# Kernel tuning notes

Measured on AMD Instinct MI355X. Metric: run time of the kernel, lower is better.

The kernel has to match this reference:

```python
import jax, jax.numpy as jnp
import numpy as np

B, N, M = 8, 8192, 2048
C1, C2 = 128, 256
H = 256  # mlp hidden/out channels


def setup_inputs() -> dict:
    key = jax.random.key(0)
    ks = jax.random.split(key, 8)
    return {
        "unknown": jax.random.normal(ks[0], (B, N, 3), dtype=jnp.float32),
        "known": jax.random.normal(ks[1], (B, M, 3), dtype=jnp.float32),
        "unknow_feats": jax.random.normal(ks[2], (B, C1, N), dtype=jnp.float32),
        "known_feats": jax.random.normal(ks[3], (B, C2, M), dtype=jnp.float32),
        "W1": jax.random.normal(ks[4], (H, C1 + C2), dtype=jnp.float32) * 0.02,
        "b1": jnp.zeros((H,), dtype=jnp.float32),
        "W2": jax.random.normal(ks[5], (H, H), dtype=jnp.float32) * 0.02,
        "b2": jnp.zeros((H,), dtype=jnp.float32),
    }


def _three_nn(unknown, known):
    # squared pairwise distances (B, n, m)
    d2 = jnp.sum((unknown[:, :, None, :] - known[:, None, :, :]) ** 2, axis=-1)
    neg_d2_top, idx = jax.lax.top_k(-d2, 3)  # 3 smallest distances
    dist = jnp.sqrt(jnp.maximum(-neg_d2_top, 0.0))  # (B, n, 3)
    return dist, idx


def _three_interpolate(features, idx, weight):
    # features: (B, c, m); idx, weight: (B, n, 3) -> (B, c, n)
    Bc, c, m = features.shape
    n = idx.shape[1]
    idx_flat = jnp.broadcast_to(idx.reshape(Bc, 1, n * 3), (Bc, c, n * 3))
    gathered = jnp.take_along_axis(features, idx_flat, axis=2).reshape(Bc, c, n, 3)
    return jnp.sum(gathered * weight[:, None, :, :], axis=-1)


def reference(unknown, known, unknow_feats, known_feats, W1, b1, W2, b2):
    dist, idx = _three_nn(unknown, known)
    dist_recip = 1.0 / (dist + 1e-8)
    weight = dist_recip / jnp.sum(dist_recip, axis=2, keepdims=True)  # (B, n, 3)
    interpolated = _three_interpolate(known_feats, idx, weight)  # (B, C2, n)
    new_features = jnp.concatenate([interpolated, unknow_feats], axis=1)  # (B, C1+C2, n)
    # shared MLP: two conv1x1 (bias, no BN) + ReLU
    h = jax.nn.relu(jnp.einsum('oc,bcn->bon', W1, new_features) + b1[None, :, None])
    out = jax.nn.relu(jnp.einsum('oc,bcn->bon', W2, h) + b2[None, :, None])
    return out
```

## Files before the change

### kernel.cpp

```cpp
#include <hip/hip_runtime.h>

using bf16x8 = __attribute__((ext_vector_type(8))) short;
using f32x4  = __attribute__((ext_vector_type(4))) float;
using f32x2  = __attribute__((ext_vector_type(2))) float;

constexpr int Bb = 8, Nn = 8192, Mm = 2048, C1 = 128, C2 = 256, Hh = 256, K1 = 384;
constexpr int KT1 = K1 / 32;
constexpr int KT2 = Hh / 32;
constexpr int RT = Hh / 16;
constexpr int NQ = 4;
constexpr int MQ = Mm / NQ;

__device__ __forceinline__ short f2bf(float x) {
  union { float f; unsigned u; } v; v.f = x;
  unsigned r = v.u + 0x7fff + ((v.u >> 16) & 1);
  return (short)(r >> 16);
}

__device__ __forceinline__ unsigned pk2bf(float a, float b) {
#if defined(__has_builtin) && __has_builtin(__builtin_amdgcn_cvt_pk_bf16_f32)
  typedef __attribute__((ext_vector_type(2))) __bf16 bf2_t;
  bf2_t r = __builtin_amdgcn_cvt_pk_bf16_f32(a, b);
  union { bf2_t v; unsigned u; } cvt; cvt.v = r;
  return cvt.u;
#else
  return (unsigned)(unsigned short)f2bf(a) | ((unsigned)(unsigned short)f2bf(b) << 16);
#endif
}

__device__ __forceinline__ float bflo(unsigned d) { return __uint_as_float(d << 16); }
__device__ __forceinline__ float bfhi(unsigned d) { return __uint_as_float(d & 0xffff0000u); }

__device__ __forceinline__ f32x2 pk_add(f32x2 a, f32x2 b) {
  f32x2 d; asm("v_pk_add_f32 %0, %1, %2" : "=v"(d) : "v"(a), "v"(b)); return d;
}
__device__ __forceinline__ f32x2 pk_mul(f32x2 a, f32x2 b) {
  f32x2 d; asm("v_pk_mul_f32 %0, %1, %2" : "=v"(d) : "v"(a), "v"(b)); return d;
}
__device__ __forceinline__ f32x2 pk_fma(f32x2 a, f32x2 b, f32x2 c) {
  f32x2 d; asm("v_pk_fma_f32 %0, %1, %2, %3" : "=v"(d) : "v"(a), "v"(b), "v"(c)); return d;
}

__device__ __forceinline__ void merge3(float a0, float a1, float a2, int A0, int A1, int A2,
                                       float b0, float b1, float b2, int B0, int B1, int B2,
                                       float& m0, float& m1, float& m2,
                                       int& j0, int& j1, int& j2) {
  bool ta = a0 <= b0;
  m0 = ta ? a0 : b0; j0 = ta ? A0 : B0;
  float na0 = ta ? a1 : a0, na1 = ta ? a2 : a1;
  int   nA0 = ta ? A1 : A0, nA1 = ta ? A2 : A1;
  float nb0 = ta ? b0 : b1, nb1 = ta ? b1 : b2;
  int   nB0 = ta ? B0 : B1, nB1 = ta ? B1 : B2;
  ta = na0 <= nb0;
  m1 = ta ? na0 : nb0; j1 = ta ? nA0 : nB0;
  float ma0 = ta ? na1 : na0; int mA0 = ta ? nA1 : nA0;
  float mb0 = ta ? nb0 : nb1; int mB0 = ta ? nB0 : nB1;
  ta = ma0 <= mb0;
  m2 = ta ? ma0 : mb0; j2 = ta ? mA0 : mB0;
}

__global__ __launch_bounds__(256) void prep_all_k(const float* __restrict__ kf,
                                                  short* __restrict__ kfTb,
                                                  const float* __restrict__ W1,
                                                  const float* __restrict__ W2,
                                                  short* __restrict__ W1f,
                                                  short* __restrict__ W2f) {
  __shared__ float tile[32][33];
  int bid = blockIdx.x, tid = threadIdx.x;
  if (bid < 4096) {
    int cx = bid & 63, ry = (bid >> 6) & 7, z = bid >> 9;
    const float* src = kf + (size_t)z * C2 * Mm;
    short* dst = kfTb + (size_t)z * Mm * C2;
    int c0 = cx * 32, r0 = ry * 32;
    int tx = tid & 31, ty = tid >> 5;
#pragma unroll
    for (int rr = ty; rr < 32; rr += 8)
      tile[rr][tx] = src[(size_t)(r0 + rr) * Mm + c0 + tx];
    __syncthreads();
#pragma unroll
    for (int cc = ty; cc < 32; cc += 8)
      dst[(size_t)(c0 + cc) * C2 + r0 + tx] = f2bf(tile[tx][cc]);
    return;
  }
  int id = (bid - 4096) * 256 + tid;
  const int n1 = KT1 * RT * 64;
  const int n2 = KT2 * RT * 64;
  if (id < n1) {
    int lane = id & 63, t = id >> 6;
    int kt = t / RT, rt = t % RT;
    int m = rt * 16 + (lane & 15), k0 = kt * 32 + (lane >> 4) * 8;
    bf16x8 f;
#pragma unroll
    for (int j = 0; j < 8; ++j) f[j] = f2bf(W1[(size_t)m * K1 + k0 + j]);
    *(bf16x8*)(W1f + (size_t)id * 8) = f;
  } else if (id < n1 + n2) {
    int id2 = id - n1;
    int lane = id2 & 63, t = id2 >> 6;
    int kt = t / RT, rt = t % RT;
    int m = rt * 16 + (lane & 15), k0 = kt * 32 + (lane >> 4) * 8;
    bf16x8 f;
#pragma unroll
    for (int j = 0; j < 8; ++j) f[j] = f2bf(W2[(size_t)m * Hh + k0 + j]);
    *(bf16x8*)(W2f + (size_t)id2 * 8) = f;
  }
}

__global__ __launch_bounds__(256) void nn_quarter_k(const float* __restrict__ unknown,
                                                    const float* __restrict__ known,
                                                    float* __restrict__ pd,
                                                    int* __restrict__ pi) {
  __shared__ float kx[MQ], ky[MQ], kz[MQ];
  int bid = blockIdx.x;
  int b = bid >> 7, rem = bid & 127;
  int q = rem & 3, nblk = rem >> 2;
  int n = nblk * 256 + threadIdx.x;
  const float* kb = known + ((size_t)b * Mm + q * MQ) * 3;
  for (int p = threadIdx.x; p < MQ; p += 256) {
    kx[p] = kb[3 * p]; ky[p] = kb[3 * p + 1]; kz[p] = kb[3 * p + 2];
  }
  __syncthreads();

  size_t ui = ((size_t)b * Nn + n) * 3;
  float ux = unknown[ui], uy = unknown[ui + 1], uz = unknown[ui + 2];
  float d0 = 1e30f, d1 = 1e30f, d2 = 1e30f;
  int i0 = 0, i1 = 0, i2 = 0;
  int gbase = q * MQ;

  f32x2 nux = { -ux, -ux }, nuy = { -uy, -uy }, nuz = { -uz, -uz };

#define NN_INS(dd, qq)                                                  \
  {                                                                     \
    if (__any((dd) < d2)) {  \
      int jm = gbase + jb + (qq);                                       \
      bool c0 = (dd) < d0, c1 = (dd) < d1, c2 = (dd) < d2;              \
      d2 = c1 ? d1 : (c2 ? (dd) : d2); i2 = c1 ? i1 : (c2 ? jm : i2);   \
      d1 = c0 ? d0 : (c1 ? (dd) : d1); i1 = c0 ? i0 : (c1 ? jm : i1);   \
      d0 = c0 ? (dd) : d0;             i0 = c0 ? jm : i0;               \
    }                                                                   \
  }

  const f32x2* kx2 = (const f32x2*)kx;
  const f32x2* ky2 = (const f32x2*)ky;
  const f32x2* kz2 = (const f32x2*)kz;
  for (int jb = 0; jb < MQ; jb += 4) {
    int h = jb >> 1;
    f32x2 xa = kx2[h], xb = kx2[h + 1];
    f32x2 ya = ky2[h], yb = ky2[h + 1];
    f32x2 za = kz2[h], zb = kz2[h + 1];
    f32x2 dxa = pk_add(xa, nux), dya = pk_add(ya, nuy), dza = pk_add(za, nuz);
    f32x2 dda = pk_fma(dza, dza, pk_fma(dya, dya, pk_mul(dxa, dxa)));
    f32x2 dxb = pk_add(xb, nux), dyb = pk_add(yb, nuy), dzb = pk_add(zb, nuz);
    f32x2 ddb = pk_fma(dzb, dzb, pk_fma(dyb, dyb, pk_mul(dxb, dxb)));
    NN_INS(dda.x, 0)
    NN_INS(dda.y, 1)
    NN_INS(ddb.x, 2)
    NN_INS(ddb.y, 3)
  }
#undef NN_INS

  size_t o = (((size_t)b * Nn + n) * NQ + q) * 3;
  pd[o] = d0; pd[o + 1] = d1; pd[o + 2] = d2;
  pi[o] = i0; pi[o + 1] = i1; pi[o + 2] = i2;
}

__global__ __launch_bounds__(256) void fused_gemm_k(
    const float* __restrict__ uf, const short* __restrict__ kfTb,
    const short* __restrict__ W1f, const float* __restrict__ b1,
    const short* __restrict__ W2f, const float* __restrict__ b2,
    const float* __restrict__ pd, const int* __restrict__ pi,
    float* __restrict__ out) {
  __shared__ short Fs[KT2 * 4 * 64 * 8];
  short* Hs = Fs;
  int bid = blockIdx.x;
  int b = bid >> 7, bt = bid & 127;
  int tid = threadIdx.x, lane = tid & 63, wv = tid >> 6;
  int quad = lane >> 4, col = lane & 15;
  const int nq = bt * 64 + wv * 16 + col;

  float w0, w1, w2;
  int g0, g1, g2;
  {
    size_t pbase = (size_t)(b * Nn + nq) * (NQ * 3);
    float4 da = *(const float4*)&pd[pbase];
    float4 db = *(const float4*)&pd[pbase + 4];
    float4 dc = *(const float4*)&pd[pbase + 8];
    int4 ia = *(const int4*)&pi[pbase];
    int4 ib = *(const int4*)&pi[pbase + 4];
    int4 ic = *(const int4*)&pi[pbase + 8];
    float t0, t1, t2, u0, u1, u2, m0, m1, m2;
    int T0, T1, T2, U0, U1, U2;
    merge3(da.x, da.y, da.z, ia.x, ia.y, ia.z,
           da.w, db.x, db.y, ia.w, ib.x, ib.y, t0, t1, t2, T0, T1, T2);
    merge3(db.z, db.w, dc.x, ib.z, ib.w, ic.x,
           dc.y, dc.z, dc.w, ic.y, ic.z, ic.w, u0, u1, u2, U0, U1, U2);
    merge3(t0, t1, t2, T0, T1, T2, u0, u1, u2, U0, U1, U2,
           m0, m1, m2, g0, g1, g2);
    float s0 = sqrtf(m0), s1 = sqrtf(m1), s2 = sqrtf(m2);
    float r0 = 1.f / (s0 + 1e-8f), r1 = 1.f / (s1 + 1e-8f), r2 = 1.f / (s2 + 1e-8f);
    float rs = 1.f / (r0 + r1 + r2);
    w0 = r0 * rs; w1 = r1 * rs; w2 = r2 * rs;
  }
  const short* kfb = kfTb + (size_t)b * Mm * C2;

#define PACK_STORE(q0, q1, q2, plane)                                         \
  {                                                                           \
    float e0 = w0 * bflo((q0).x) + w1 * bflo((q1).x) + w2 * bflo((q2).x);     \
    float e1 = w0 * bfhi((q0).x) + w1 * bfhi((q1).x) + w2 * bfhi((q2).x);     \
    float e2 = w0 * bflo((q0).y) + w1 * bflo((q1).y) + w2 * bflo((q2).y);     \
    float e3 = w0 * bfhi((q0).y) + w1 * bfhi((q1).y) + w2 * bfhi((q2).y);     \
    float e4 = w0 * bflo((q0).z) + w1 * bflo((q1).z) + w2 * bflo((q2).z);     \
    float e5 = w0 * bfhi((q0).z) + w1 * bfhi((q1).z) + w2 * bfhi((q2).z);     \
    float e6 = w0 * bflo((q0).w) + w1 * bflo((q1).w) + w2 * bflo((q2).w);     \
    float e7 = w0 * bfhi((q0).w) + w1 * bfhi((q1).w) + w2 * bfhi((q2).w);     \
    uint4 packed;                                                             \
    packed.x = pk2bf(e0, e1); packed.y = pk2bf(e2, e3);                       \
    packed.z = pk2bf(e4, e5); packed.w = pk2bf(e6, e7);                       \
    *(uint4*)&Fs[(((plane) * 4 + wv) * 64 + lane) * 8] = packed;              \
  }

#define GATHER_KT(kt, plane)                                                  \
  {                                                                           \
    int c0 = (kt) * 32 + quad * 8;                                            \
    uint4 q0 = *(const uint4*)&kfb[(size_t)g0 * C2 + c0];                     \
    uint4 q1 = *(const uint4*)&kfb[(size_t)g1 * C2 + c0];                     \
    uint4 q2 = *(const uint4*)&kfb[(size_t)g2 * C2 + c0];                     \
    PACK_STORE(q0, q1, q2, plane)                                             \
  }

#pragma unroll 3
  for (int kt = 0; kt < 6; ++kt) GATHER_KT(kt, kt)
  __syncthreads();

  uint4 pf0, pf1, pf2, pf3, pf4, pf5;
  {
    int c06 = 6 * 32 + quad * 8, c07 = 7 * 32 + quad * 8;
    pf0 = *(const uint4*)&kfb[(size_t)g0 * C2 + c06];
    pf1 = *(const uint4*)&kfb[(size_t)g1 * C2 + c06];
    pf2 = *(const uint4*)&kfb[(size_t)g2 * C2 + c06];
    pf3 = *(const uint4*)&kfb[(size_t)g0 * C2 + c07];
    pf4 = *(const uint4*)&kfb[(size_t)g1 * C2 + c07];
    pf5 = *(const uint4*)&kfb[(size_t)g2 * C2 + c07];
  }

  f32x4 acc[4][4];
#pragma unroll
  for (int r = 0; r < 4; ++r)
#pragma unroll
    for (int c = 0; c < 4; ++c) acc[r][c] = (f32x4){0.f, 0.f, 0.f, 0.f};

  for (int kt = 0; kt < 6; ++kt) {
    bf16x8 Afr[4], Bfr[4];
#pragma unroll
    for (int r = 0; r < 4; ++r)
      Afr[r] = *(const bf16x8*)(W1f + ((size_t)(kt * RT + wv * 4 + r) * 64 + lane) * 8);
#pragma unroll
    for (int c = 0; c < 4; ++c)
      Bfr[c] = *(const bf16x8*)&Fs[((kt * 4 + c) * 64 + lane) * 8];
#pragma unroll
    for (int r = 0; r < 4; ++r)
#pragma unroll
      for (int c = 0; c < 4; ++c)
        acc[r][c] = __builtin_amdgcn_mfma_f32_16x16x32_bf16(Afr[r], Bfr[c], acc[r][c], 0, 0, 0);
  }
  __syncthreads();

  float eu[4][8];
#pragma unroll
  for (int kt = 8; kt < 12; ++kt) {
    int c1 = (kt - 8) * 32 + quad * 8;
#pragma unroll
    for (int j = 0; j < 8; ++j)
      eu[kt - 8][j] = uf[((size_t)b * C1 + c1 + j) * Nn + nq];
  }
  PACK_STORE(pf0, pf1, pf2, 0)
  PACK_STORE(pf3, pf4, pf5, 1)
#pragma unroll
  for (int kt = 8; kt < 12; ++kt) {
    uint4 packed;
    packed.x = pk2bf(eu[kt - 8][0], eu[kt - 8][1]);
    packed.y = pk2bf(eu[kt - 8][2], eu[kt - 8][3]);
    packed.z = pk2bf(eu[kt - 8][4], eu[kt - 8][5]);
    packed.w = pk2bf(eu[kt - 8][6], eu[kt - 8][7]);
    *(uint4*)&Fs[(((kt - 6) * 4 + wv) * 64 + lane) * 8] = packed;
  }
#undef GATHER_KT
#undef PACK_STORE
  __syncthreads();

  for (int kt = 6; kt < KT1; ++kt) {
    bf16x8 Afr[4], Bfr[4];
#pragma unroll
    for (int r = 0; r < 4; ++r)
      Afr[r] = *(const bf16x8*)(W1f + ((size_t)(kt * RT + wv * 4 + r) * 64 + lane) * 8);
#pragma unroll
    for (int c = 0; c < 4; ++c)
      Bfr[c] = *(const bf16x8*)&Fs[(((kt - 6) * 4 + c) * 64 + lane) * 8];
#pragma unroll
    for (int r = 0; r < 4; ++r)
#pragma unroll
      for (int c = 0; c < 4; ++c)
        acc[r][c] = __builtin_amdgcn_mfma_f32_16x16x32_bf16(Afr[r], Bfr[c], acc[r][c], 0, 0, 0);
  }

#pragma unroll
  for (int r = 0; r < 4; ++r) {
    f32x4 bq = *(const f32x4*)&b1[wv * 64 + r * 16 + quad * 4];
#pragma unroll
    for (int c = 0; c < 4; ++c)
#pragma unroll
      for (int reg = 0; reg < 4; ++reg)
        acc[r][c][reg] = fmaxf(acc[r][c][reg] + bq[reg], 0.f);
  }
  __syncthreads();
  {
    int addr_lo = (((quad & 1) * 2) * 16 + col) * 4;
    bool hiSel = lane >= 32;
#pragma unroll
    for (int ktl = 0; ktl < 2; ++ktl)
#pragma unroll
      for (int c = 0; c < 4; ++c) {
        float e[8];
#pragma unroll
        for (int j = 0; j < 8; ++j) {
          int addr = addr_lo + (j >> 2) * 64;
          int lo = __builtin_amdgcn_ds_bpermute(addr, __float_as_int(acc[ktl * 2][c][j & 3]));
          int hi = __builtin_amdgcn_ds_bpermute(addr, __float_as_int(acc[ktl * 2 + 1][c][j & 3]));
          e[j] = __int_as_float(hiSel ? hi : lo);
        }
        uint4 packed;
        packed.x = pk2bf(e[0], e[1]); packed.y = pk2bf(e[2], e[3]);
        packed.z = pk2bf(e[4], e[5]); packed.w = pk2bf(e[6], e[7]);
        *(uint4*)&Hs[(((wv * 2 + ktl) * 4 + c) * 64 + lane) * 8] = packed;
      }
  }
  __syncthreads();

  f32x4 acc2[4][4];
#pragma unroll
  for (int r = 0; r < 4; ++r)
#pragma unroll
    for (int c = 0; c < 4; ++c) acc2[r][c] = (f32x4){0.f, 0.f, 0.f, 0.f};

  for (int kt = 0; kt < KT2; ++kt) {
    bf16x8 Afr[4], Bfr[4];
#pragma unroll
    for (int r = 0; r < 4; ++r)
      Afr[r] = *(const bf16x8*)(W2f + ((size_t)(kt * RT + wv * 4 + r) * 64 + lane) * 8);
#pragma unroll
    for (int c = 0; c < 4; ++c)
      Bfr[c] = *(const bf16x8*)&Hs[((kt * 4 + c) * 64 + lane) * 8];
#pragma unroll
    for (int r = 0; r < 4; ++r)
#pragma unroll
      for (int c = 0; c < 4; ++c)
        acc2[r][c] = __builtin_amdgcn_mfma_f32_16x16x32_bf16(Afr[r], Bfr[c], acc2[r][c], 0, 0, 0);
  }

#pragma unroll
  for (int r = 0; r < 4; ++r) {
    f32x4 bq = *(const f32x4*)&b2[wv * 64 + r * 16 + quad * 4];
#pragma unroll
    for (int c = 0; c < 4; ++c)
#pragma unroll
      for (int reg = 0; reg < 4; ++reg) {
        int rowg = wv * 64 + r * 16 + quad * 4 + reg;
        int n = bt * 64 + c * 16 + col;
        out[((size_t)b * Hh + rowg) * Nn + n] = fmaxf(acc2[r][c][reg] + bq[reg], 0.f);
      }
  }
}

extern "C" void kernel_launch(void* const* d_in, const int* in_sizes, int n_in,
                              void* d_out, int out_size, void* d_ws, size_t ws_size,
                              hipStream_t stream) {
  const float* unknown = (const float*)d_in[0];
  const float* known   = (const float*)d_in[1];
  const float* uf      = (const float*)d_in[2];
  const float* kf      = (const float*)d_in[3];
  const float* W1      = (const float*)d_in[4];
  const float* b1      = (const float*)d_in[5];
  const float* W2      = (const float*)d_in[6];
  const float* b2      = (const float*)d_in[7];
  float* out = (float*)d_out;

  char* p = (char*)d_ws;
  short* kfTb = (short*)p; p += (size_t)Bb * Mm * C2 * 2;
  short* W1f = (short*)p;  p += (size_t)KT1 * RT * 64 * 8 * 2;
  short* W2f = (short*)p;  p += (size_t)KT2 * RT * 64 * 8 * 2;
  float* pd  = (float*)p;  p += (size_t)Bb * Nn * NQ * 3 * 4;
  int* pi    = (int*)p;    p += (size_t)Bb * Nn * NQ * 3 * 4;

  const int prep_blocks = 4096 + (KT1 * RT * 64 + KT2 * RT * 64 + 255) / 256;
  prep_all_k<<<dim3(prep_blocks), dim3(256), 0, stream>>>(kf, kfTb, W1, W2, W1f, W2f);
  nn_quarter_k<<<dim3(Bb * 32 * NQ), dim3(256), 0, stream>>>(unknown, known, pd, pi);
  fused_gemm_k<<<dim3(Bb * (Nn / 64)), dim3(256), 0, stream>>>(
      uf, kfTb, W1f, b1, W2f, b2, pd, pi, out);
}
```

Measured before the change: 214.8 us.

## Restructure first GEMM into three 4-tile stages overlapping gathers with MFMA

The layer-1 K loop is reordered into three stages of four k-tiles. The unknown-feature tiles are loaded first and multiplied while the register-prefetched gathers for the first half of the interpolated channels are in flight. The next gather batch is then issued before the following MFMA stage. This hides the latency of the random gathers from known_feats behind matrix math, at the cost of more live registers (24 uint4 prefetch values) and an extra barrier.

```diff
diff --git a/kernel.cpp b/kernel.cpp
--- a/kernel.cpp
+++ b/kernel.cpp
@@ -177,16 +177,25 @@
   int quad = lane >> 4, col = lane & 15;
   const int nq = bt * 64 + wv * 16 + col;
 
+  size_t pbase = (size_t)(b * Nn + nq) * (NQ * 3);
+  float4 da = *(const float4*)&pd[pbase];
+  float4 db = *(const float4*)&pd[pbase + 4];
+  float4 dc = *(const float4*)&pd[pbase + 8];
+  int4 ia = *(const int4*)&pi[pbase];
+  int4 ib = *(const int4*)&pi[pbase + 4];
+  int4 ic = *(const int4*)&pi[pbase + 8];
+  float eu[4][8];
+#pragma unroll
+  for (int kt = 8; kt < 12; ++kt) {
+    int c1 = (kt - 8) * 32 + quad * 8;
+#pragma unroll
+    for (int j = 0; j < 8; ++j)
+      eu[kt - 8][j] = uf[((size_t)b * C1 + c1 + j) * Nn + nq];
+  }
+
   float w0, w1, w2;
   int g0, g1, g2;
   {
-    size_t pbase = (size_t)(b * Nn + nq) * (NQ * 3);
-    float4 da = *(const float4*)&pd[pbase];
-    float4 db = *(const float4*)&pd[pbase + 4];
-    float4 dc = *(const float4*)&pd[pbase + 8];
-    int4 ia = *(const int4*)&pi[pbase];
-    int4 ib = *(const int4*)&pi[pbase + 4];
-    int4 ic = *(const int4*)&pi[pbase + 8];
     float t0, t1, t2, u0, u1, u2, m0, m1, m2;
     int T0, T1, T2, U0, U1, U2;
     merge3(da.x, da.y, da.z, ia.x, ia.y, ia.z,
@@ -218,62 +227,6 @@
     *(uint4*)&Fs[(((plane) * 4 + wv) * 64 + lane) * 8] = packed;              \
   }
 
-#define GATHER_KT(kt, plane)                                                  \
-  {                                                                           \
-    int c0 = (kt) * 32 + quad * 8;                                            \
-    uint4 q0 = *(const uint4*)&kfb[(size_t)g0 * C2 + c0];                     \
-    uint4 q1 = *(const uint4*)&kfb[(size_t)g1 * C2 + c0];                     \
-    uint4 q2 = *(const uint4*)&kfb[(size_t)g2 * C2 + c0];                     \
-    PACK_STORE(q0, q1, q2, plane)                                             \
-  }
-
-#pragma unroll 3
-  for (int kt = 0; kt < 6; ++kt) GATHER_KT(kt, kt)
-  __syncthreads();
-
-  uint4 pf0, pf1, pf2, pf3, pf4, pf5;
-  {
-    int c06 = 6 * 32 + quad * 8, c07 = 7 * 32 + quad * 8;
-    pf0 = *(const uint4*)&kfb[(size_t)g0 * C2 + c06];
-    pf1 = *(const uint4*)&kfb[(size_t)g1 * C2 + c06];
-    pf2 = *(const uint4*)&kfb[(size_t)g2 * C2 + c06];
-    pf3 = *(const uint4*)&kfb[(size_t)g0 * C2 + c07];
-    pf4 = *(const uint4*)&kfb[(size_t)g1 * C2 + c07];
-    pf5 = *(const uint4*)&kfb[(size_t)g2 * C2 + c07];
-  }
-
-  f32x4 acc[4][4];
-#pragma unroll
-  for (int r = 0; r < 4; ++r)
-#pragma unroll
-    for (int c = 0; c < 4; ++c) acc[r][c] = (f32x4){0.f, 0.f, 0.f, 0.f};
-
-  for (int kt = 0; kt < 6; ++kt) {
-    bf16x8 Afr[4], Bfr[4];
-#pragma unroll
-    for (int r = 0; r < 4; ++r)
-      Afr[r] = *(const bf16x8*)(W1f + ((size_t)(kt * RT + wv * 4 + r) * 64 + lane) * 8);
-#pragma unroll
-    for (int c = 0; c < 4; ++c)
-      Bfr[c] = *(const bf16x8*)&Fs[((kt * 4 + c) * 64 + lane) * 8];
-#pragma unroll
-    for (int r = 0; r < 4; ++r)
-#pragma unroll
-      for (int c = 0; c < 4; ++c)
-        acc[r][c] = __builtin_amdgcn_mfma_f32_16x16x32_bf16(Afr[r], Bfr[c], acc[r][c], 0, 0, 0);
-  }
-  __syncthreads();
-
-  float eu[4][8];
-#pragma unroll
-  for (int kt = 8; kt < 12; ++kt) {
-    int c1 = (kt - 8) * 32 + quad * 8;
-#pragma unroll
-    for (int j = 0; j < 8; ++j)
-      eu[kt - 8][j] = uf[((size_t)b * C1 + c1 + j) * Nn + nq];
-  }
-  PACK_STORE(pf0, pf1, pf2, 0)
-  PACK_STORE(pf3, pf4, pf5, 1)
 #pragma unroll
   for (int kt = 8; kt < 12; ++kt) {
     uint4 packed;
@@ -281,26 +234,89 @@
     packed.y = pk2bf(eu[kt - 8][2], eu[kt - 8][3]);
     packed.z = pk2bf(eu[kt - 8][4], eu[kt - 8][5]);
     packed.w = pk2bf(eu[kt - 8][6], eu[kt - 8][7]);
-    *(uint4*)&Fs[(((kt - 6) * 4 + wv) * 64 + lane) * 8] = packed;
-  }
-#undef GATHER_KT
+    *(uint4*)&Fs[(((kt - 8) * 4 + wv) * 64 + lane) * 8] = packed;
+  }
+
+  uint4 pa0, pa1, pa2, pa3, pa4, pa5, pa6, pa7, pa8, pa9, paA, paB;
+  {
+    int c0 = 0 * 32 + quad * 8, c1 = 1 * 32 + quad * 8;
+    int c2 = 2 * 32 + quad * 8, c3 = 3 * 32 + quad * 8;
+    pa0 = *(const uint4*)&kfb[(size_t)g0 * C2 + c0];
+    pa1 = *(const uint4*)&kfb[(size_t)g1 * C2 + c0];
+    pa2 = *(const uint4*)&kfb[(size_t)g2 * C2 + c0];
+    pa3 = *(const uint4*)&kfb[(size_t)g0 * C2 + c1];
+    pa4 = *(const uint4*)&kfb[(size_t)g1 * C2 + c1];
+    pa5 = *(const uint4*)&kfb[(size_t)g2 * C2 + c1];
+    pa6 = *(const uint4*)&kfb[(size_t)g0 * C2 + c2];
+    pa7 = *(const uint4*)&kfb[(size_t)g1 * C2 + c2];
+    pa8 = *(const uint4*)&kfb[(size_t)g2 * C2 + c2];
+    pa9 = *(const uint4*)&kfb[(size_t)g0 * C2 + c3];
+    paA = *(const uint4*)&kfb[(size_t)g1 * C2 + c3];
+    paB = *(const uint4*)&kfb[(size_t)g2 * C2 + c3];
+  }
+  __syncthreads();
+
+  f32x4 acc[4][4];
+#pragma unroll
+  for (int r = 0; r < 4; ++r)
+#pragma unroll
+    for (int c = 0; c < 4; ++c) acc[r][c] = (f32x4){0.f, 0.f, 0.f, 0.f};
+
+#define K1_GEN(KTBASE)                                                        \
+  for (int ktl = 0; ktl < 4; ++ktl) {                                         \
+    int kt = (KTBASE) + ktl;                                                  \
+    bf16x8 Afr[4], Bfr[4];                                                    \
+    _Pragma("unroll")                                                         \
+    for (int r = 0; r < 4; ++r)                                               \
+      Afr[r] = *(const bf16x8*)(W1f + ((size_t)(kt * RT + wv * 4 + r) * 64 + lane) * 8); \
+    _Pragma("unroll")                                                         \
+    for (int c = 0; c < 4; ++c)                                               \
+      Bfr[c] = *(const bf16x8*)&Fs[((ktl * 4 + c) * 64 + lane) * 8];          \
+    _Pragma("unroll")                                                         \
+    for (int r = 0; r < 4; ++r)                                               \
+      _Pragma("unroll")                                                       \
+      for (int c = 0; c < 4; ++c)                                             \
+        acc[r][c] = __builtin_amdgcn_mfma_f32_16x16x32_bf16(Afr[r], Bfr[c], acc[r][c], 0, 0, 0); \
+  }
+
+  K1_GEN(8)
+  __syncthreads();
+
+  PACK_STORE(pa0, pa1, pa2, 0)
+  PACK_STORE(pa3, pa4, pa5, 1)
+  PACK_STORE(pa6, pa7, pa8, 2)
+  PACK_STORE(pa9, paA, paB, 3)
+  uint4 pb0, pb1, pb2, pb3, pb4, pb5, pb6, pb7, pb8, pb9, pbA, pbB;
+  {
+    int c4 = 4 * 32 + quad * 8, c5 = 5 * 32 + quad * 8;
+    int c6 = 6 * 32 + quad * 8, c7 = 7 * 32 + quad * 8;
+    pb0 = *(const uint4*)&kfb[(size_t)g0 * C2 + c4];
+    pb1 = *(const uint4*)&kfb[(size_t)g1 * C2 + c4];
+    pb2 = *(const uint4*)&kfb[(size_t)g2 * C2 + c4];
+    pb3 = *(const uint4*)&kfb[(size_t)g0 * C2 + c5];
+    pb4 = *(const uint4*)&kfb[(size_t)g1 * C2 + c5];
+    pb5 = *(const uint4*)&kfb[(size_t)g2 * C2 + c5];
+    pb6 = *(const uint4*)&kfb[(size_t)g0 * C2 + c6];
+    pb7 = *(const uint4*)&kfb[(size_t)g1 * C2 + c6];
+    pb8 = *(const uint4*)&kfb[(size_t)g2 * C2 + c6];
+    pb9 = *(const uint4*)&kfb[(size_t)g0 * C2 + c7];
+    pbA = *(const uint4*)&kfb[(size_t)g1 * C2 + c7];
+    pbB = *(const uint4*)&kfb[(size_t)g2 * C2 + c7];
+  }
+  __syncthreads();
+
+  K1_GEN(0)
+  __syncthreads();
+
+  PACK_STORE(pb0, pb1, pb2, 0)
+  PACK_STORE(pb3, pb4, pb5, 1)
+  PACK_STORE(pb6, pb7, pb8, 2)
+  PACK_STORE(pb9, pbA, pbB, 3)
+  __syncthreads();
+
+  K1_GEN(4)
+#undef K1_GEN
 #undef PACK_STORE
-  __syncthreads();
-
-  for (int kt = 6; kt < KT1; ++kt) {
-    bf16x8 Afr[4], Bfr[4];
-#pragma unroll
-    for (int r = 0; r < 4; ++r)
-      Afr[r] = *(const bf16x8*)(W1f + ((size_t)(kt * RT + wv * 4 + r) * 64 + lane) * 8);
-#pragma unroll
-    for (int c = 0; c < 4; ++c)
-      Bfr[c] = *(const bf16x8*)&Fs[(((kt - 6) * 4 + c) * 64 + lane) * 8];
-#pragma unroll
-    for (int r = 0; r < 4; ++r)
-#pragma unroll
-      for (int c = 0; c < 4; ++c)
-        acc[r][c] = __builtin_amdgcn_mfma_f32_16x16x32_bf16(Afr[r], Bfr[c], acc[r][c], 0, 0, 0);
-  }
 
 #pragma unroll
   for (int r = 0; r < 4; ++r) {
```

Measured after the change: 211.5 us. No clear change (-1.5%).
